# Optimization experiments

Hardware: AMD Instinct MI355X
Metric: run time of the kernel (lower is better)

Reference implementation:

```python
import jax, jax.numpy as jnp
import numpy as np

E = 2048      # embedding_size
H = 16        # num_heads
D = 128       # head_dim
G = 4         # gqa_factor
KH = H // G   # kv heads
F = 8192      # up_proj_size
B, S = 2, 2048


def _layer_norm(x, g, b, eps=1e-5):
    mu = jnp.mean(x, axis=-1, keepdims=True)
    var = jnp.mean(jnp.square(x - mu), axis=-1, keepdims=True)
    return (x - mu) * jax.lax.rsqrt(var + eps) * g + b


def setup_inputs() -> dict:
    key = jax.random.key(0)
    ks = jax.random.split(key, 16)
    std = 0.02
    inp = {
        'x': jax.random.normal(ks[0], (B, S, E), dtype=jnp.float32),
        'ln1_g': jnp.ones((E,), jnp.float32),
        'ln1_b': jnp.zeros((E,), jnp.float32),
        'wq': jax.random.normal(ks[1], (E, H * D), jnp.float32) * std,
        'bq': jnp.zeros((H * D,), jnp.float32),
        'wk': jax.random.normal(ks[2], (E, KH * D), jnp.float32) * std,
        'bk': jnp.zeros((KH * D,), jnp.float32),
        'wv': jax.random.normal(ks[3], (E, KH * D), jnp.float32) * std,
        'bv': jnp.zeros((KH * D,), jnp.float32),
        'wo': jax.random.normal(ks[4], (H * D, E), jnp.float32) * std,
        'bo': jnp.zeros((E,), jnp.float32),
        'ln2_g': jnp.ones((E,), jnp.float32),
        'ln2_b': jnp.zeros((E,), jnp.float32),
        'wu': jax.random.normal(ks[5], (E, F), jnp.float32) * std,
        'bu': jnp.zeros((F,), jnp.float32),
        'wd': jax.random.normal(ks[6], (F, E), jnp.float32) * std,
        'bd': jnp.zeros((E,), jnp.float32),
    }
    return inp


def _block(x, ln1_g, ln1_b, wq, bq, wk, bk, wv, bv, wo, bo, ln2_g, ln2_b, wu, bu, wd, bd):
    b, s, e = x.shape
    # attention sub-block (use_cache=False, train_mode=False -> no dropout)
    x1 = _layer_norm(x, ln1_g, ln1_b)
    q = (x1 @ wq + bq).reshape(b, s, H, D).transpose(0, 2, 1, 3)       # (B,H,S,D)
    q = q.reshape(b, KH, G, s, D)                                       # (B,KH,G,S,D)
    k = (x1 @ wk + bk).reshape(b, s, KH, D).transpose(0, 2, 1, 3)      # (B,KH,S,D)
    v = (x1 @ wv + bv).reshape(b, s, KH, D).transpose(0, 2, 1, 3)      # (B,KH,S,D)
    scores = jnp.einsum('bkgsd,bktd->bkgst', q, k) / np.sqrt(D).astype(np.float32)
    causal = jnp.tril(jnp.ones((s, s), dtype=bool))                     # True = keep
    scores = jnp.where(causal, scores, -jnp.inf)
    att = jax.nn.softmax(scores, axis=-1)
    o = jnp.einsum('bkgst,bktd->bkgsd', att, v)                         # (B,KH,G,S,D)
    o = o.reshape(b, H, s, D).transpose(0, 2, 1, 3).reshape(b, s, H * D)
    x = x + (o @ wo + bo)
    # MLP sub-block
    x2 = _layer_norm(x, ln2_g, ln2_b)
    h = jax.nn.gelu(x2 @ wu + bu, approximate=False)
    x = x + (h @ wd + bd)
    return x


def reference(x, ln1_g, ln1_b, wq, bq, wk, bk, wv, bv, wo, bo, ln2_g, ln2_b, wu, bu, wd, bd):
    return _block(x, ln1_g, ln1_b, wq, bq, wk, bk, wv, bv, wo, bo, ln2_g, ln2_b, wu, bu, wd, bd)
```

## Files before the change

kernel.cpp:

```cpp
#include <hip/hip_runtime.h>
#include <hip/hip_bf16.h>
#include <cstdint>
#include <math.h>

typedef unsigned short u16;
using f32x4   = __attribute__((ext_vector_type(4))) float;
using short8  = __attribute__((ext_vector_type(8))) short;
using short4v = __attribute__((ext_vector_type(4))) short;

#define DEV static __device__ __forceinline__

DEV u16 f2bf(float f) {
  union { float f; unsigned u; } v; v.f = f;
  unsigned r = v.u + 0x7fffu + ((v.u >> 16) & 1u);
  return (u16)(r >> 16);
}

DEV f32x4 mfma_bf16(short8 a, short8 b, f32x4 c) {
  return __builtin_amdgcn_mfma_f32_16x16x32_bf16(a, b, c, 0, 0, 0);
}

DEV void gload16(const void* g, void* l) {
  __builtin_amdgcn_global_load_lds((const __attribute__((address_space(1))) void*)g,
                                   (__attribute__((address_space(3))) void*)l,
                                   16, 0, 0);
}

__global__ __launch_bounds__(256) void prep_kernel(
    const float* __restrict__ x, const float* __restrict__ g,
    const float* __restrict__ bt, u16* __restrict__ x1,
    const float* __restrict__ wq, const float* __restrict__ wk,
    const float* __restrict__ wv, const float* __restrict__ wo,
    const float* __restrict__ wu, const float* __restrict__ wd,
    u16* __restrict__ wqT, u16* __restrict__ wkT, u16* __restrict__ wvT,
    u16* __restrict__ woT, u16* __restrict__ wuT, u16* __restrict__ wdT)
{
  __shared__ float sm[32 * 33];
  int bid = blockIdx.x;
  const int t = threadIdx.x;

  if (bid < 4096) {
    const int lane = t & 63, w = t >> 6;
    const float* xr = x + (size_t)bid * 2048 + t * 8;
    float v[8];
    {
      const float4* p4 = (const float4*)xr;
      float4 a = p4[0], b = p4[1];
      v[0] = a.x; v[1] = a.y; v[2] = a.z; v[3] = a.w;
      v[4] = b.x; v[5] = b.y; v[6] = b.z; v[7] = b.w;
    }
    float s = 0.f;
#pragma unroll
    for (int j = 0; j < 8; j++) s += v[j];
#pragma unroll
    for (int m = 1; m < 64; m <<= 1) s += __shfl_xor(s, m);
    if (lane == 0) sm[w] = s;
    __syncthreads();
    const float mu = (sm[0] + sm[1] + sm[2] + sm[3]) * (1.f / 2048.f);
    float q = 0.f;
#pragma unroll
    for (int j = 0; j < 8; j++) { v[j] -= mu; q += v[j] * v[j]; }
#pragma unroll
    for (int m = 1; m < 64; m <<= 1) q += __shfl_xor(q, m);
    if (lane == 0) sm[4 + w] = q;
    __syncthreads();
    const float rstd = rsqrtf((sm[4] + sm[5] + sm[6] + sm[7]) * (1.f / 2048.f) + 1e-5f);
    const float4* g4 = (const float4*)(g + t * 8);
    const float4* b4 = (const float4*)(bt + t * 8);
    float4 ga = g4[0], gb = g4[1], ba = b4[0], bb = b4[1];
    float gg[8] = {ga.x, ga.y, ga.z, ga.w, gb.x, gb.y, gb.z, gb.w};
    float bbv[8] = {ba.x, ba.y, ba.z, ba.w, bb.x, bb.y, bb.z, bb.w};
    short8 o;
#pragma unroll
    for (int j = 0; j < 8; j++) o[j] = (short)f2bf(v[j] * rstd * gg[j] + bbv[j]);
    *(short8*)&x1[(size_t)bid * 2048 + t * 8] = o;
    return;
  }
  bid -= 4096;

  const float* in; u16* outp; int K, N, bx, by;
  if (bid < 4096)              { in = wq; outp = wqT; K = 2048; N = 2048; bx = bid & 63;  by = bid >> 6; }
  else if ((bid -= 4096) < 1024)  { in = wk; outp = wkT; K = 2048; N = 512;  bx = bid & 15;  by = bid >> 4; }
  else if ((bid -= 1024) < 1024)  { in = wv; outp = wvT; K = 2048; N = 512;  bx = bid & 15;  by = bid >> 4; }
  else if ((bid -= 1024) < 4096)  { in = wo; outp = woT; K = 2048; N = 2048; bx = bid & 63;  by = bid >> 6; }
  else if ((bid -= 4096) < 16384) { in = wu; outp = wuT; K = 2048; N = 8192; bx = bid & 255; by = bid >> 8; }
  else { bid -= 16384;            in = wd; outp = wdT; K = 8192; N = 2048; bx = bid & 63;  by = bid >> 6; }

  const int n0 = bx * 32, k0 = by * 32;
  {
    const int c = t & 31, r = t >> 5;
#pragma unroll
    for (int i = 0; i < 4; i++)
      sm[(r + i * 8) * 33 + c] = in[(size_t)(k0 + r + i * 8) * N + n0 + c];
  }
  __syncthreads();
  {
    const int c4 = (t & 7) * 4, r = t >> 3;
    short4v o;
#pragma unroll
    for (int j = 0; j < 4; j++) o[j] = (short)f2bf(sm[(c4 + j) * 33 + r]);
    *(short4v*)&outp[(size_t)(n0 + r) * K + k0 + c4] = o;
  }
}

__global__ __launch_bounds__(256) void ln_kernel(
    const float* __restrict__ x, const float* __restrict__ g,
    const float* __restrict__ bt, u16* __restrict__ out)
{
  __shared__ float red1[4], red2[4];
  const int row = blockIdx.x;
  const int t = threadIdx.x;
  const int lane = t & 63, w = t >> 6;
  const float* xr = x + (size_t)row * 2048 + t * 8;
  float v[8];
  {
    const float4* p4 = (const float4*)xr;
    float4 a = p4[0], b = p4[1];
    v[0] = a.x; v[1] = a.y; v[2] = a.z; v[3] = a.w;
    v[4] = b.x; v[5] = b.y; v[6] = b.z; v[7] = b.w;
  }
  float s = 0.f;
#pragma unroll
  for (int j = 0; j < 8; j++) s += v[j];
#pragma unroll
  for (int m = 1; m < 64; m <<= 1) s += __shfl_xor(s, m);
  if (lane == 0) red1[w] = s;
  __syncthreads();
  const float mu = (red1[0] + red1[1] + red1[2] + red1[3]) * (1.f / 2048.f);
  float q = 0.f;
#pragma unroll
  for (int j = 0; j < 8; j++) { v[j] -= mu; q += v[j] * v[j]; }
#pragma unroll
  for (int m = 1; m < 64; m <<= 1) q += __shfl_xor(q, m);
  if (lane == 0) red2[w] = q;
  __syncthreads();
  const float rstd = rsqrtf((red2[0] + red2[1] + red2[2] + red2[3]) * (1.f / 2048.f) + 1e-5f);
  const float4* g4 = (const float4*)(g + t * 8);
  const float4* b4 = (const float4*)(bt + t * 8);
  float4 ga = g4[0], gb = g4[1], ba = b4[0], bb = b4[1];
  float gg[8] = {ga.x, ga.y, ga.z, ga.w, gb.x, gb.y, gb.z, gb.w};
  float bbv[8] = {ba.x, ba.y, ba.z, ba.w, bb.x, bb.y, bb.z, bb.w};
  short8 o;
#pragma unroll
  for (int j = 0; j < 8; j++) o[j] = (short)f2bf(v[j] * rstd * gg[j] + bbv[j]);
  *(short8*)&out[(size_t)row * 2048 + t * 8] = o;
}

template<int MODE, int N, int K, int STRIPE_N>
__global__ void __launch_bounds__(256) gemm_sb(
    const u16* __restrict__ A, const u16* __restrict__ Bt,
    const float* __restrict__ b0, const float* __restrict__ b1,
    const float* __restrict__ b2, const float* __restrict__ resid,
    u16* __restrict__ o0, u16* __restrict__ o1, u16* __restrict__ o2,
    float* __restrict__ of)
{
  __shared__ u16 As[128 * 64];
  __shared__ u16 Bs[128 * 64];
  constexpr int TN = N / 128;

  const int bid = blockIdx.x;
  const int xcd = bid & 7, wl = bid >> 3;
  int m0, n0;
  if constexpr (STRIPE_N) {
    constexpr int NSTR = TN / 8;
    n0 = (xcd * NSTR + (wl % NSTR)) * 128;
    m0 = (wl / NSTR) * 128;
  } else {
    m0 = (xcd * 4 + (wl & 3)) * 128;
    n0 = (wl >> 2) * 128;
  }
  const int tid = threadIdx.x;
  const int lane = tid & 63, w = tid >> 6;
  const int wm = w >> 1, wn = w & 1;
  const int z = lane >> 4, l15 = lane & 15;

  f32x4 acc[4][4];
#pragma unroll
  for (int m = 0; m < 4; m++)
#pragma unroll
    for (int n = 0; n < 4; n++)
#pragma unroll
      for (int i = 0; i < 4; i++) acc[m][n][i] = 0.f;

  for (int k0 = 0; k0 < K; k0 += 64) {
#pragma unroll
    for (int j = 0; j < 4; j++) {
      const int seg = w * 4 + j;
      const int c = seg * 64 + lane;
      const int r = c >> 3;
      const int cc = (c & 7) ^ (r & 7);
      gload16(A + (size_t)(m0 + r) * K + k0 + cc * 8, &As[seg * 512]);
    }
#pragma unroll
    for (int j = 0; j < 4; j++) {
      const int seg = w * 4 + j;
      const int c = seg * 64 + lane;
      const int r = c >> 3;
      const int cc = (c & 7) ^ (r & 7);
      gload16(Bt + (size_t)(n0 + r) * K + k0 + cc * 8, &Bs[seg * 512]);
    }
    asm volatile("s_waitcnt vmcnt(0)" ::: "memory");
    __syncthreads();

#pragma unroll
    for (int kk = 0; kk < 2; kk++) {
      short8 af[4], bfr[4];
#pragma unroll
      for (int m = 0; m < 4; m++) {
        const int row = wm * 64 + m * 16 + l15;
        const int off = row * 64 + ((kk * 32 + z * 8) ^ ((row & 7) << 3));
        af[m] = *(const short8*)&As[off];
      }
#pragma unroll
      for (int n = 0; n < 4; n++) {
        const int row = wn * 64 + n * 16 + l15;
        const int off = row * 64 + ((kk * 32 + z * 8) ^ ((row & 7) << 3));
        bfr[n] = *(const short8*)&Bs[off];
      }
      __builtin_amdgcn_s_setprio(1);
#pragma unroll
      for (int m = 0; m < 4; m++)
#pragma unroll
        for (int n = 0; n < 4; n++)
          acc[m][n] = mfma_bf16(af[m], bfr[n], acc[m][n]);
      __builtin_amdgcn_s_setprio(0);
    }
    __syncthreads();
  }

#pragma unroll
  for (int m = 0; m < 4; m++) {
    const int row0 = m0 + wm * 64 + m * 16 + z * 4;
#pragma unroll
    for (int n = 0; n < 4; n++) {
      const int col = n0 + wn * 64 + n * 16 + l15;
      f32x4 v = acc[m][n];
      if constexpr (MODE == 6) {
        if (col < 2048) {
          const float bb = b0[col];
#pragma unroll
          for (int i = 0; i < 4; i++)
            o0[(size_t)(row0 + i) * 2048 + col] = f2bf((v[i] + bb) * 0.08838834764831845f);
        } else if (col < 2560) {
          const int ck = col - 2048;
          const float bb = b1[ck];
#pragma unroll
          for (int i = 0; i < 4; i++)
            o1[(size_t)(row0 + i) * 512 + ck] = f2bf(v[i] + bb);
        } else {
          const int cc = col - 2560;
          const float bb = b2[cc];
          const int kh = cc >> 7, d = cc & 127;
          const int bidx = row0 >> 11, sidx = row0 & 2047;
          u16* vrow = &o2[((size_t)(bidx * 4 + kh) * 128 + d) * 2048 + sidx];
          short4v pq;
#pragma unroll
          for (int i = 0; i < 4; i++) pq[i] = (short)f2bf(v[i] + bb);
          *(short4v*)vrow = pq;
        }
      } else {
        const float bb = b0[col];
        if constexpr (MODE == 3) {
#pragma unroll
          for (int i = 0; i < 4; i++) {
            const size_t idx = (size_t)(row0 + i) * N + col;
            of[idx] = v[i] + bb + resid[idx];
          }
        } else if constexpr (MODE == 4) {
#pragma unroll
          for (int i = 0; i < 4; i++) {
            const float xx = v[i] + bb;
            o0[(size_t)(row0 + i) * N + col] =
                f2bf(0.5f * xx * (1.f + erff(xx * 0.70710678118654752f)));
          }
        } else {
#pragma unroll
          for (int i = 0; i < 4; i++) {
            const size_t idx = (size_t)(row0 + i) * N + col;
            of[idx] = v[i] + bb + of[idx];
          }
        }
      }
    }
  }
}

__global__ void __launch_bounds__(256) attn_kernel(
    const u16* __restrict__ qb, const u16* __restrict__ kb,
    const u16* __restrict__ vt, u16* __restrict__ ob)
{
  __shared__ u16 Kt[2][64 * 128];
  __shared__ u16 Vs[2][128 * 64];
  __shared__ u16 Pl[4 * 32 * 64];

  const int idx = blockIdx.x;
  const int xcd = idx & 7;
  const int u = (idx >> 3) & 31;
  const int half = idx >> 8;
  const int bh = xcd * 4 + (u & 3);
  const int qh = u >> 2;
  const int qt = half ? (15 - qh) : qh;

  const int b = bh >> 4, h = bh & 15, kh = h >> 2;
  const int q0 = qt * 128;
  const int tid = threadIdx.x, lane = tid & 63, w = tid >> 6;
  const int z = lane >> 4, l15 = lane & 15;
  const int qw0 = q0 + w * 32;
  const int ksw = (l15 & 7) << 3;

  short8 qf[2][4];
#pragma unroll
  for (int m = 0; m < 2; m++)
#pragma unroll
    for (int kk = 0; kk < 4; kk++)
      qf[m][kk] = *(const short8*)&qb[(size_t)(b * 2048 + qw0 + m * 16 + l15) * 2048 +
                                      h * 128 + kk * 32 + z * 8];

  f32x4 oacc[2][8];
#pragma unroll
  for (int m = 0; m < 2; m++)
#pragma unroll
    for (int n = 0; n < 8; n++)
#pragma unroll
      for (int i = 0; i < 4; i++) oacc[m][n][i] = 0.f;
  float mst[2][4], lst[2][4];
#pragma unroll
  for (int m = 0; m < 2; m++)
#pragma unroll
    for (int i = 0; i < 4; i++) { mst[m][i] = -1e30f; lst[m][i] = 0.f; }

  auto STAGE = [&](int tt, int bufsel) {
    const int kv0s = tt * 64;
#pragma unroll
    for (int j = 0; j < 4; j++) {
      const int seg = w * 4 + j;
      const int c = seg * 64 + lane;
      const int r = c >> 4;
      const int cc = (c & 15) ^ (r & 7);
      gload16(kb + (size_t)(b * 2048 + kv0s + r) * 512 + kh * 128 + cc * 8,
              &Kt[bufsel][seg * 512]);
    }
#pragma unroll
    for (int j = 0; j < 4; j++) {
      const int seg = w * 4 + j;
      const int c = seg * 64 + lane;
      const int d = c >> 3;
      const int cc = (c & 7) ^ (d & 7);
      gload16(vt + (size_t)((b * 4 + kh) * 128 + d) * 2048 + kv0s + cc * 8,
              &Vs[bufsel][seg * 512]);
    }
  };

  const int ntiles = q0 / 64 + 2;

  STAGE(0, 0);
  asm volatile("s_waitcnt vmcnt(0)" ::: "memory");
  __syncthreads();

  for (int t = 0; t < ntiles; t++) {
    const int cur = t & 1;
    if (t + 1 < ntiles) STAGE(t + 1, cur ^ 1);

    const int kv0 = t * 64;
    if (kv0 <= qw0 + 31) {
      f32x4 sf[2][4];
#pragma unroll
      for (int m = 0; m < 2; m++)
#pragma unroll
        for (int n = 0; n < 4; n++)
#pragma unroll
          for (int i = 0; i < 4; i++) sf[m][n][i] = 0.f;

      __builtin_amdgcn_s_setprio(1);
#pragma unroll
      for (int kk = 0; kk < 4; kk++) {
        short8 kfr[4];
#pragma unroll
        for (int n = 0; n < 4; n++) {
          const int row = n * 16 + l15;
          kfr[n] = *(const short8*)&Kt[cur][row * 128 + ((kk * 32 + z * 8) ^ ksw)];
        }
#pragma unroll
        for (int m = 0; m < 2; m++)
#pragma unroll
          for (int n = 0; n < 4; n++)
            sf[m][n] = mfma_bf16(qf[m][kk], kfr[n], sf[m][n]);
      }
      __builtin_amdgcn_s_setprio(0);

      u16* Pw = &Pl[w * 2048];
      const bool edge = (kv0 + 63 > qw0);
#pragma unroll
      for (int m = 0; m < 2; m++) {
#pragma unroll
        for (int i = 0; i < 4; i++) {
          const int rq = qw0 + m * 16 + z * 4 + i;
          if (edge) {
#pragma unroll
            for (int n = 0; n < 4; n++)
              if (kv0 + n * 16 + l15 > rq) sf[m][n][i] = -1e30f;
          }
          float mx = fmaxf(fmaxf(sf[m][0][i], sf[m][1][i]), fmaxf(sf[m][2][i], sf[m][3][i]));
          mx = fmaxf(mx, __shfl_xor(mx, 1));
          mx = fmaxf(mx, __shfl_xor(mx, 2));
          mx = fmaxf(mx, __shfl_xor(mx, 4));
          mx = fmaxf(mx, __shfl_xor(mx, 8));
          const bool grow = mx > mst[m][i];
          const float mn = grow ? mx : mst[m][i];
          float rs = 0.f;
#pragma unroll
          for (int n = 0; n < 4; n++) {
            const float p = __expf(sf[m][n][i] - mn);
            sf[m][n][i] = p;
            rs += p;
          }
          rs += __shfl_xor(rs, 1);
          rs += __shfl_xor(rs, 2);
          rs += __shfl_xor(rs, 4);
          rs += __shfl_xor(rs, 8);
          if (grow) {
            const float al = __expf(mst[m][i] - mx);
            mst[m][i] = mx;
            lst[m][i] = lst[m][i] * al + rs;
#pragma unroll
            for (int n = 0; n < 8; n++) oacc[m][n][i] *= al;
          } else {
            lst[m][i] += rs;
          }
          const int prow = m * 16 + z * 4 + i;
          const int psw = ((z * 4 + i) & 7) << 3;
#pragma unroll
          for (int n = 0; n < 4; n++)
            Pw[prow * 64 + ((n * 16 + l15) ^ psw)] = f2bf(sf[m][n][i]);
        }
      }

      __builtin_amdgcn_s_setprio(1);
#pragma unroll
      for (int kk = 0; kk < 2; kk++) {
        short8 af[2], vf[8];
#pragma unroll
        for (int m = 0; m < 2; m++) {
          const int row = m * 16 + l15;
          af[m] = *(const short8*)&Pw[row * 64 + ((kk * 32 + z * 8) ^ ksw)];
        }
#pragma unroll
        for (int n = 0; n < 8; n++) {
          const int row = n * 16 + l15;
          vf[n] = *(const short8*)&Vs[cur][row * 64 + ((kk * 32 + z * 8) ^ ksw)];
        }
#pragma unroll
        for (int m = 0; m < 2; m++)
#pragma unroll
          for (int n = 0; n < 8; n++)
            oacc[m][n] = mfma_bf16(af[m], vf[n], oacc[m][n]);
      }
      __builtin_amdgcn_s_setprio(0);
    }

    asm volatile("s_waitcnt vmcnt(0)" ::: "memory");
    __syncthreads();
  }

#pragma unroll
  for (int m = 0; m < 2; m++)
#pragma unroll
    for (int i = 0; i < 4; i++) {
      const float inv = 1.0f / lst[m][i];
      const int rq = qw0 + m * 16 + z * 4 + i;
      u16* orow = &ob[(size_t)(b * 2048 + rq) * 2048 + h * 128];
#pragma unroll
      for (int n = 0; n < 8; n++)
        orow[n * 16 + l15] = f2bf(oacc[m][n][i] * inv);
    }
}

extern "C" void kernel_launch(void* const* d_in, const int* in_sizes, int n_in,
                              void* d_out, int out_size, void* d_ws, size_t ws_size,
                              hipStream_t stream) {
  (void)in_sizes; (void)n_in; (void)out_size; (void)ws_size;
  const float* x     = (const float*)d_in[0];
  const float* ln1_g = (const float*)d_in[1];
  const float* ln1_b = (const float*)d_in[2];
  const float* wq    = (const float*)d_in[3];
  const float* bq    = (const float*)d_in[4];
  const float* wk    = (const float*)d_in[5];
  const float* bk    = (const float*)d_in[6];
  const float* wv    = (const float*)d_in[7];
  const float* bv    = (const float*)d_in[8];
  const float* wo    = (const float*)d_in[9];
  const float* bo    = (const float*)d_in[10];
  const float* ln2_g = (const float*)d_in[11];
  const float* ln2_b = (const float*)d_in[12];
  const float* wu    = (const float*)d_in[13];
  const float* bu    = (const float*)d_in[14];
  const float* wd    = (const float*)d_in[15];
  const float* bd    = (const float*)d_in[16];
  float* out = (float*)d_out;

  char* p = (char*)d_ws;
  u16* wqT = (u16*)p; p += (size_t)2048 * 2048 * 2;
  u16* wkT = (u16*)p; p += (size_t)512 * 2048 * 2;
  u16* wvT = (u16*)p; p += (size_t)512 * 2048 * 2;
  u16* woT = (u16*)p; p += (size_t)2048 * 2048 * 2;
  u16* wuT = (u16*)p; p += (size_t)8192 * 2048 * 2;
  u16* wdT = (u16*)p; p += (size_t)2048 * 8192 * 2;
  u16* x1  = (u16*)p; p += (size_t)4096 * 2048 * 2;
  u16* qbuf= (u16*)p; p += (size_t)4096 * 2048 * 2;
  u16* kbuf= (u16*)p; p += (size_t)4096 * 512 * 2;
  u16* vtb = (u16*)p; p += (size_t)4096 * 512 * 2;
  u16* hb  = (u16*)p; p += (size_t)4096 * 8192 * 2;
  u16* ob  = x1;
  u16* x2  = qbuf;

  prep_kernel<<<47104, 256, 0, stream>>>(
      x, ln1_g, ln1_b, x1, wq, wk, wv, wo, wu, wd,
      wqT, wkT, wvT, woT, wuT, wdT);

  gemm_sb<6, 3072, 2048, 0><<<768, 256, 0, stream>>>(
      x1, wqT, bq, bk, bv, nullptr, qbuf, kbuf, vtb, nullptr);

  attn_kernel<<<512, 256, 0, stream>>>(qbuf, kbuf, vtb, ob);

  gemm_sb<3, 2048, 2048, 0><<<512, 256, 0, stream>>>(
      ob, woT, bo, nullptr, nullptr, x, nullptr, nullptr, nullptr, out);

  ln_kernel<<<4096, 256, 0, stream>>>(out, ln2_g, ln2_b, x2);

  gemm_sb<4, 8192, 2048, 1><<<2048, 256, 0, stream>>>(
      x2, wuT, bu, nullptr, nullptr, nullptr, hb, nullptr, nullptr, nullptr);
  gemm_sb<5, 2048, 8192, 1><<<512, 256, 0, stream>>>(
      hb, wdT, bd, nullptr, nullptr, nullptr, nullptr, nullptr, nullptr, out);
}
```

Measured before the change: 714.9 us.

## Add triple-buffered GEMM kernel with XCD striping for MLP projections

```diff
diff --git a/kernel.cpp b/kernel.cpp
--- a/kernel.cpp
+++ b/kernel.cpp
@@ -260,25 +260,126 @@
         }
       } else {
         const float bb = b0[col];
-        if constexpr (MODE == 3) {
-#pragma unroll
-          for (int i = 0; i < 4; i++) {
-            const size_t idx = (size_t)(row0 + i) * N + col;
-            of[idx] = v[i] + bb + resid[idx];
-          }
-        } else if constexpr (MODE == 4) {
-#pragma unroll
-          for (int i = 0; i < 4; i++) {
-            const float xx = v[i] + bb;
-            o0[(size_t)(row0 + i) * N + col] =
-                f2bf(0.5f * xx * (1.f + erff(xx * 0.70710678118654752f)));
-          }
-        } else {
-#pragma unroll
-          for (int i = 0; i < 4; i++) {
-            const size_t idx = (size_t)(row0 + i) * N + col;
-            of[idx] = v[i] + bb + of[idx];
-          }
+#pragma unroll
+        for (int i = 0; i < 4; i++) {
+          const size_t idx = (size_t)(row0 + i) * N + col;
+          of[idx] = v[i] + bb + resid[idx];
+        }
+      }
+    }
+  }
+}
+
+template<int MODE, int N, int K, int STRIPE_N>
+__global__ void __launch_bounds__(256) gemm_p3(
+    const u16* __restrict__ A, const u16* __restrict__ Bt,
+    const float* __restrict__ b0,
+    u16* __restrict__ o0, float* __restrict__ of)
+{
+  __shared__ u16 As[3][128 * 32];
+  __shared__ u16 Bs[3][128 * 32];
+  constexpr int TN = N / 128;
+  constexpr int NT = K / 32;
+
+  const int bid = blockIdx.x;
+  const int xcd = bid & 7, wl = bid >> 3;
+  int m0, n0;
+  if constexpr (STRIPE_N) {
+    constexpr int NSTR = TN / 8;
+    n0 = (xcd * NSTR + (wl % NSTR)) * 128;
+    m0 = (wl / NSTR) * 128;
+  } else {
+    m0 = (xcd * 4 + (wl & 3)) * 128;
+    n0 = (wl >> 2) * 128;
+  }
+  const int tid = threadIdx.x;
+  const int lane = tid & 63, w = tid >> 6;
+  const int wm = w >> 1, wn = w & 1;
+  const int z = lane >> 4, l15 = lane & 15;
+
+  f32x4 acc[4][4];
+#pragma unroll
+  for (int m = 0; m < 4; m++)
+#pragma unroll
+    for (int n = 0; n < 4; n++)
+#pragma unroll
+      for (int i = 0; i < 4; i++) acc[m][n][i] = 0.f;
+
+  auto stage = [&](int g) {
+    const int sl = g % 3;
+    const int kc = g * 32;
+#pragma unroll
+    for (int s = 0; s < 2; s++) {
+      const int c = s * 256 + tid;
+      const int r = c >> 2, q = c & 3;
+      const int cg = q ^ ((r >> 1) & 3);
+      gload16(A + (size_t)(m0 + r) * K + kc + cg * 8, &As[sl][c * 8]);
+    }
+#pragma unroll
+    for (int s = 0; s < 2; s++) {
+      const int c = s * 256 + tid;
+      const int r = c >> 2, q = c & 3;
+      const int cg = q ^ ((r >> 1) & 3);
+      gload16(Bt + (size_t)(n0 + r) * K + kc + cg * 8, &Bs[sl][c * 8]);
+    }
+  };
+
+  stage(0); stage(1);
+  asm volatile("s_waitcnt vmcnt(4)" ::: "memory");
+  __syncthreads();
+
+  for (int t = 0; t < NT; t++) {
+    const int sl = t % 3;
+    if (t + 2 < NT) stage(t + 2);
+
+    short8 af[4], bfr[4];
+#pragma unroll
+    for (int m = 0; m < 4; m++) {
+      const int row = wm * 64 + m * 16 + l15;
+      af[m] = *(const short8*)&As[sl][row * 32 + ((z ^ ((row >> 1) & 3)) * 8)];
+    }
+#pragma unroll
+    for (int n = 0; n < 4; n++) {
+      const int row = wn * 64 + n * 16 + l15;
+      bfr[n] = *(const short8*)&Bs[sl][row * 32 + ((z ^ ((row >> 1) & 3)) * 8)];
+    }
+    __builtin_amdgcn_s_setprio(1);
+#pragma unroll
+    for (int m = 0; m < 4; m++)
+#pragma unroll
+      for (int n = 0; n < 4; n++)
+        acc[m][n] = mfma_bf16(af[m], bfr[n], acc[m][n]);
+    __builtin_amdgcn_s_setprio(0);
+
+    if (t + 2 < NT) {
+      asm volatile("s_waitcnt vmcnt(4)" ::: "memory");
+      __syncthreads();
+    } else if (t + 1 < NT) {
+      asm volatile("s_waitcnt vmcnt(0)" ::: "memory");
+      __syncthreads();
+    }
+  }
+
+#pragma unroll
+  for (int m = 0; m < 4; m++) {
+    const int row0 = m0 + wm * 64 + m * 16 + z * 4;
+#pragma unroll
+    for (int n = 0; n < 4; n++) {
+      const int col = n0 + wn * 64 + n * 16 + l15;
+      f32x4 v = acc[m][n];
+      const float bb = b0[col];
+      if constexpr (MODE == 4) {
+#pragma unroll
+        for (int i = 0; i < 4; i++) {
+          const float xx = v[i] + bb;
+          o0[(size_t)(row0 + i) * N + col] =
+              f2bf(0.5f * xx * (1.f + erff(xx * 0.70710678118654752f)));
+        }
+      } else {
+#pragma unroll
+        for (int i = 0; i < 4; i++) {
+          const size_t idx = (size_t)(row0 + i) * N + col;
+          of[idx] = v[i] + bb + of[idx];
         }
       }
     }
@@ -527,8 +628,6 @@
 
   ln_kernel<<<4096, 256, 0, stream>>>(out, ln2_g, ln2_b, x2);
 
-  gemm_sb<4, 8192, 2048, 1><<<2048, 256, 0, stream>>>(
-      x2, wuT, bu, nullptr, nullptr, nullptr, hb, nullptr, nullptr, nullptr);
-  gemm_sb<5, 2048, 8192, 1><<<512, 256, 0, stream>>>(
-      hb, wdT, bd, nullptr, nullptr, nullptr, nullptr, nullptr, nullptr, out);
-}
+  gemm_p3<4, 8192, 2048, 1><<<2048, 256, 0, stream>>>(x2, wuT, bu, hb, nullptr);
+  gemm_p3<5, 2048, 8192, 1><<<512, 256, 0, stream>>>(hb, wdT, bd, nullptr, out);
+}
```

Result: slower. 776.0 us (+8.5%).
